# Performance work log

Measured on AMD Instinct MI355X. Metric: run time of the kernel, lower is better.

The kernel has to match this reference:

```python
import jax, jax.numpy as jnp
import numpy as np

GROUP_SIZE = 128
QMIN, QMAX = -128.0, 127.0  # int8
EPS = 1.1920928955078125e-07  # float32 eps, guards zero scale


def setup_inputs() -> dict:
    key = jax.random.key(0)
    x = jax.random.normal(key, (8192, 8192), dtype=jnp.float32)
    return {"x": x}


def reference(x):
    # Dynamic per-group min/max observer + asymmetric int8 fake quantize.
    n, k = x.shape
    xg = x.reshape(n, k // GROUP_SIZE, GROUP_SIZE)  # [n, n_groups, g]
    # Observer: min/max per group, always including zero (asymmetric affine)
    mn = jnp.minimum(jnp.min(xg, axis=-1, keepdims=True), 0.0)
    mx = jnp.maximum(jnp.max(xg, axis=-1, keepdims=True), 0.0)
    scale = jnp.maximum((mx - mn) / (QMAX - QMIN), EPS)
    zero_point = jnp.clip(jnp.round(QMIN - mn / scale), QMIN, QMAX)  # int32 zp as float
    # scaled_fake_quantize: quantize -> clamp -> dequantize (round half-even)
    q = jnp.clip(jnp.round(xg / scale) + zero_point, QMIN, QMAX)
    return ((q - zero_point) * scale).reshape(n, k)
```

## Files before the change

### kernel.cpp

```cpp
#include <hip/hip_runtime.h>


typedef float f32x4 __attribute__((ext_vector_type(4)));

constexpr float QMIN = -128.0f;
constexpr float QMAX = 127.0f;
constexpr float EPSF = 1.1920928955078125e-07f;

__device__ __forceinline__ float min4(f32x4 v) {
  return fminf(fminf(v.x, v.y), fminf(v.z, v.w));
}
__device__ __forceinline__ float max4(f32x4 v) {
  return fmaxf(fmaxf(v.x, v.y), fmaxf(v.z, v.w));
}

__global__ __launch_bounds__(256) void dsq_kernel(
    const float* __restrict__ x, float* __restrict__ out, int n16) {
  const f32x4* __restrict__ x4 = reinterpret_cast<const f32x4*>(x);
  f32x4* __restrict__ o4 = reinterpret_cast<f32x4*>(out);

  int t = blockIdx.x * blockDim.x + threadIdx.x;
  int nthreads = gridDim.x * blockDim.x;

  for (int p = t; p < n16; p += nthreads) {
    int base = ((p >> 3) << 5) + (p & 7);
    f32x4 v0 = x4[base];
    f32x4 v1 = x4[base + 8];
    f32x4 v2 = x4[base + 16];
    f32x4 v3 = x4[base + 24];

    float mn = fminf(fminf(min4(v0), min4(v1)), fminf(min4(v2), min4(v3)));
    float mx = fmaxf(fmaxf(max4(v0), max4(v1)), fmaxf(max4(v2), max4(v3)));

    #pragma unroll
    for (int m = 1; m < 8; m <<= 1) {
      mn = fminf(mn, __shfl_xor(mn, m, 64));
      mx = fmaxf(mx, __shfl_xor(mx, m, 64));
    }

    mn = fminf(mn, 0.0f);
    mx = fmaxf(mx, 0.0f);

    float scale = fmaxf((mx - mn) * (1.0f / 255.0f), EPSF);
    float inv = 1.0f / scale;
    float zp = fminf(fmaxf(rintf(QMIN - mn / scale), QMIN), QMAX);
    float nzs = -zp * scale;

    f32x4 o0, o1, o2, o3;
    #define QDQ(e) fmaf(fminf(fmaxf(rintf((e) * inv) + zp, QMIN), QMAX), scale, nzs)
    o0.x = QDQ(v0.x); o0.y = QDQ(v0.y); o0.z = QDQ(v0.z); o0.w = QDQ(v0.w);
    o1.x = QDQ(v1.x); o1.y = QDQ(v1.y); o1.z = QDQ(v1.z); o1.w = QDQ(v1.w);
    o2.x = QDQ(v2.x); o2.y = QDQ(v2.y); o2.z = QDQ(v2.z); o2.w = QDQ(v2.w);
    o3.x = QDQ(v3.x); o3.y = QDQ(v3.y); o3.z = QDQ(v3.z); o3.w = QDQ(v3.w);
    #undef QDQ

    __builtin_nontemporal_store(o0, &o4[base]);
    __builtin_nontemporal_store(o1, &o4[base + 8]);
    __builtin_nontemporal_store(o2, &o4[base + 16]);
    __builtin_nontemporal_store(o3, &o4[base + 24]);
  }
}

extern "C" void kernel_launch(void* const* d_in, const int* in_sizes, int n_in,
                              void* d_out, int out_size, void* d_ws, size_t ws_size,
                              hipStream_t stream) {
  const float* x = (const float*)d_in[0];
  float* out = (float*)d_out;
  int n16 = out_size / 16;

  dsq_kernel<<<2048, 256, 0, stream>>>(x, out, n16);
}
```

Before: 440.5 us.

## Software-pipeline group loads with 16 lanes per group and 8 floats per lane

Each quantization group is now spread over 16 lanes holding 8 floats each, instead of 8 lanes holding 16, and the reduction uses four shuffle steps. The grid-stride loop is software-pipelined so the next iteration's loads are issued before the current group is reduced, quantized and stored, to hide memory latency. The zero-point division is also replaced with an FMA by the reciprocal. The trade-off is one more shuffle step per group and extra registers for the prefetched data, and the reciprocal form can differ from the reference in rare rounding cases.

```diff
diff --git a/kernel.cpp b/kernel.cpp
--- a/kernel.cpp
+++ b/kernel.cpp
@@ -14,51 +14,56 @@
   return fmaxf(fmaxf(v.x, v.y), fmaxf(v.z, v.w));
 }
 
+__device__ __forceinline__ void process_store(f32x4 v0, f32x4 v1,
+                                              f32x4* __restrict__ o4, int i0) {
+  float mn = fminf(min4(v0), min4(v1));
+  float mx = fmaxf(max4(v0), max4(v1));
+
+  #pragma unroll
+  for (int m = 1; m < 16; m <<= 1) {
+    mn = fminf(mn, __shfl_xor(mn, m, 64));
+    mx = fmaxf(mx, __shfl_xor(mx, m, 64));
+  }
+
+  mn = fminf(mn, 0.0f);
+  mx = fmaxf(mx, 0.0f);
+
+  float scale = fmaxf((mx - mn) * (1.0f / 255.0f), EPSF);
+  float inv = 1.0f / scale;
+  float zp = fminf(fmaxf(rintf(fmaf(-mn, inv, QMIN)), QMIN), QMAX);
+  float nzs = -zp * scale;
+
+  f32x4 o0, o1;
+  #define QDQ(e) fmaf(fminf(fmaxf(rintf((e) * inv) + zp, QMIN), QMAX), scale, nzs)
+  o0.x = QDQ(v0.x); o0.y = QDQ(v0.y); o0.z = QDQ(v0.z); o0.w = QDQ(v0.w);
+  o1.x = QDQ(v1.x); o1.y = QDQ(v1.y); o1.z = QDQ(v1.z); o1.w = QDQ(v1.w);
+  #undef QDQ
+
+  __builtin_nontemporal_store(o0, &o4[i0]);
+  __builtin_nontemporal_store(o1, &o4[i0 + 16]);
+}
+
 __global__ __launch_bounds__(256) void dsq_kernel(
-    const float* __restrict__ x, float* __restrict__ out, int n16) {
+    const float* __restrict__ x, float* __restrict__ out, int n8) {
   const f32x4* __restrict__ x4 = reinterpret_cast<const f32x4*>(x);
   f32x4* __restrict__ o4 = reinterpret_cast<f32x4*>(out);
 
   int t = blockIdx.x * blockDim.x + threadIdx.x;
   int nthreads = gridDim.x * blockDim.x;
+  if (t >= n8) return;
 
-  for (int p = t; p < n16; p += nthreads) {
-    int base = ((p >> 3) << 5) + (p & 7);
-    f32x4 v0 = x4[base];
-    f32x4 v1 = x4[base + 8];
-    f32x4 v2 = x4[base + 16];
-    f32x4 v3 = x4[base + 24];
+  int i0 = ((t >> 4) << 5) + (t & 15);
+  f32x4 c0 = x4[i0];
+  f32x4 c1 = x4[i0 + 16];
 
-    float mn = fminf(fminf(min4(v0), min4(v1)), fminf(min4(v2), min4(v3)));
-    float mx = fmaxf(fmaxf(max4(v0), max4(v1)), fmaxf(max4(v2), max4(v3)));
-
-    #pragma unroll
-    for (int m = 1; m < 8; m <<= 1) {
-      mn = fminf(mn, __shfl_xor(mn, m, 64));
-      mx = fmaxf(mx, __shfl_xor(mx, m, 64));
-    }
-
-    mn = fminf(mn, 0.0f);
-    mx = fmaxf(mx, 0.0f);
-
-    float scale = fmaxf((mx - mn) * (1.0f / 255.0f), EPSF);
-    float inv = 1.0f / scale;
-    float zp = fminf(fmaxf(rintf(QMIN - mn / scale), QMIN), QMAX);
-    float nzs = -zp * scale;
-
-    f32x4 o0, o1, o2, o3;
-    #define QDQ(e) fmaf(fminf(fmaxf(rintf((e) * inv) + zp, QMIN), QMAX), scale, nzs)
-    o0.x = QDQ(v0.x); o0.y = QDQ(v0.y); o0.z = QDQ(v0.z); o0.w = QDQ(v0.w);
-    o1.x = QDQ(v1.x); o1.y = QDQ(v1.y); o1.z = QDQ(v1.z); o1.w = QDQ(v1.w);
-    o2.x = QDQ(v2.x); o2.y = QDQ(v2.y); o2.z = QDQ(v2.z); o2.w = QDQ(v2.w);
-    o3.x = QDQ(v3.x); o3.y = QDQ(v3.y); o3.z = QDQ(v3.z); o3.w = QDQ(v3.w);
-    #undef QDQ
-
-    __builtin_nontemporal_store(o0, &o4[base]);
-    __builtin_nontemporal_store(o1, &o4[base + 8]);
-    __builtin_nontemporal_store(o2, &o4[base + 16]);
-    __builtin_nontemporal_store(o3, &o4[base + 24]);
+  for (int p = t + nthreads; p < n8; p += nthreads) {
+    int i1 = ((p >> 4) << 5) + (p & 15);
+    f32x4 nx0 = x4[i1];
+    f32x4 nx1 = x4[i1 + 16];
+    process_store(c0, c1, o4, i0);
+    c0 = nx0; c1 = nx1; i0 = i1;
   }
+  process_store(c0, c1, o4, i0);
 }
 
 extern "C" void kernel_launch(void* const* d_in, const int* in_sizes, int n_in,
@@ -66,7 +71,7 @@
                               hipStream_t stream) {
   const float* x = (const float*)d_in[0];
   float* out = (float*)d_out;
-  int n16 = out_size / 16;
+  int n8 = out_size / 8;
 
-  dsq_kernel<<<2048, 256, 0, stream>>>(x, out, n16);
+  dsq_kernel<<<2048, 256, 0, stream>>>(x, out, n8);
 }
```

Result: no change. 443.5 us (+0.7%).
